# Kernel tuning notes

Measured on AMD Instinct MI355X. Metric: run time of the kernel, lower is better.

## Reference

```python
import jax, jax.numpy as jnp
import numpy as np

LORA_ALPHA = 2.0

def setup_inputs() -> dict:
    key = jax.random.key(0)
    k1, k2, k3, k4 = jax.random.split(key, 4)
    B, S, D_IN, D_OUT, R = 4, 2048, 4096, 4096, 16
    x = jax.random.normal(k1, (B, S, D_IN), dtype=jnp.float32)
    weight = jax.random.normal(k2, (D_OUT, D_IN), dtype=jnp.float32) * (1.0 / np.sqrt(D_IN))
    lora_A = jax.random.normal(k3, (R, D_IN), dtype=jnp.float32) * (1.0 / np.sqrt(D_IN))
    lora_B = jax.random.normal(k4, (D_OUT, R), dtype=jnp.float32) * 0.02
    return {"x": x, "weight": weight, "lora_A": lora_A, "lora_B": lora_B}

def reference(x, weight, lora_A, lora_B):
    # main_out = F.linear(x, weight) = x @ weight.T
    main_out = jnp.einsum('bsd,od->bso', x, weight)
    # Faithful to source: materialize lora_weight = B @ A (out x in), then full linear
    lora_weight = lora_B @ lora_A  # [out, in]
    lora_out = jnp.einsum('bsd,od->bso', x, lora_weight) * LORA_ALPHA
    return main_out + lora_out
```

## Files before the change

kernel.cpp:

```cpp
#include <hip/hip_runtime.h>
#include <stdint.h>

typedef __attribute__((ext_vector_type(8))) short bf16x8;
typedef __attribute__((ext_vector_type(4))) float f32x4;

#define GM 8192
#define GN 4096
#define GK 4096
#define KTILES (GK / 64)

__device__ __forceinline__ unsigned short f2bf(float f) {
  union { float f; unsigned int u; } c; c.f = f;
  unsigned int u = c.u;
  unsigned int r = u + 0x7FFFu + ((u >> 16) & 1u);
  return (unsigned short)(r >> 16);
}

__global__ __launch_bounds__(256) void cvt_x_kernel(const float* __restrict__ x,
                                                    unsigned short* __restrict__ xb) {
  int i = blockIdx.x * 256 + threadIdx.x;
  const float4* p = (const float4*)x + (size_t)i * 2;
  float4 a = p[0], b = p[1];
  unsigned short t[8] = { f2bf(a.x), f2bf(a.y), f2bf(a.z), f2bf(a.w),
                          f2bf(b.x), f2bf(b.y), f2bf(b.z), f2bf(b.w) };
  int4 pk; __builtin_memcpy(&pk, t, 16);
  ((int4*)xb)[i] = pk;
}

__global__ __launch_bounds__(256) void weff_kernel(const float* __restrict__ w,
                                                   const float* __restrict__ lA,
                                                   const float* __restrict__ lB,
                                                   unsigned short* __restrict__ wb) {
  const int K = GK;
  int idx = blockIdx.x * 256 + threadIdx.x;
  int cg = idx & 511;
  int rg = idx >> 9;
  int i0 = cg << 3;
  int o0 = rg << 3;

  float acc[8][8];
#pragma unroll
  for (int r = 0; r < 8; ++r)
#pragma unroll
    for (int c = 0; c < 8; ++c) acc[r][c] = 0.f;

#pragma unroll
  for (int r = 0; r < 16; ++r) {
    float4 a0 = *(const float4*)(lA + (size_t)r * K + i0);
    float4 a1 = *(const float4*)(lA + (size_t)r * K + i0 + 4);
    float av[8] = { a0.x, a0.y, a0.z, a0.w, a1.x, a1.y, a1.z, a1.w };
#pragma unroll
    for (int row = 0; row < 8; ++row) {
      float b = lB[(size_t)(o0 + row) * 16 + r];
#pragma unroll
      for (int c = 0; c < 8; ++c) acc[row][c] += b * av[c];
    }
  }

#pragma unroll
  for (int row = 0; row < 8; ++row) {
    float4 w0 = *(const float4*)(w + (size_t)(o0 + row) * K + i0);
    float4 w1 = *(const float4*)(w + (size_t)(o0 + row) * K + i0 + 4);
    unsigned short t[8] = {
      f2bf(w0.x + 2.0f * acc[row][0]), f2bf(w0.y + 2.0f * acc[row][1]),
      f2bf(w0.z + 2.0f * acc[row][2]), f2bf(w0.w + 2.0f * acc[row][3]),
      f2bf(w1.x + 2.0f * acc[row][4]), f2bf(w1.y + 2.0f * acc[row][5]),
      f2bf(w1.z + 2.0f * acc[row][6]), f2bf(w1.w + 2.0f * acc[row][7]) };
    int4 pk; __builtin_memcpy(&pk, t, 16);
    *(int4*)(wb + (size_t)(o0 + row) * K + i0) = pk;
  }
}


__device__ __forceinline__ void gload16(const unsigned short* g, char* l) {
  __builtin_amdgcn_global_load_lds((__attribute__((address_space(1))) void*)g,
                                   (__attribute__((address_space(3))) void*)l, 16, 0, 0);
}

__device__ __forceinline__ void bar() {
  asm volatile("" ::: "memory");
  __builtin_amdgcn_s_barrier();
  asm volatile("" ::: "memory");
}

template <int N>
__device__ __forceinline__ void vmwait() {
  if constexpr (N == 0)      asm volatile("s_waitcnt vmcnt(0)" ::: "memory");
  else if constexpr (N == 2) asm volatile("s_waitcnt vmcnt(2)" ::: "memory");
  else if constexpr (N == 4) asm volatile("s_waitcnt vmcnt(4)" ::: "memory");
  else if constexpr (N == 6) asm volatile("s_waitcnt vmcnt(6)" ::: "memory");
}

#define MFMA_BF16(a, b, c) __builtin_amdgcn_mfma_f32_16x16x32_bf16((a), (b), (c), 0, 0, 0)

template <int HALF>
__device__ __forceinline__ void stage_half(const unsigned short* A, const unsigned short* B,
                                           char* smem, int bm0, int bn0, int w, int lane,
                                           int kt, int buf) {
  int sr, isB;
  if constexpr (HALF == 0)      { sr = w + (w & 4);                   isB = 0; }
  else if constexpr (HALF == 1) { sr = ((w >> 1) << 2) + (w & 1);     isB = 1; }
  else if constexpr (HALF == 2) { sr = ((w >> 1) << 2) + (w & 1) + 2; isB = 1; }
  else                          { sr = w + (w & 4) + 4;               isB = 0; }
  const unsigned short* mat = isB ? B : A;
  const int grow = (isB ? bn0 : bm0) + sr * 16 + (lane >> 2);
  const int gcol = ((lane & 3) * 8) ^ ((lane & 32) ? 16 : 0);
#pragma unroll
  for (int sc = 0; sc < 2; ++sc) {
    const unsigned short* src = mat + (size_t)grow * GK + kt * 64 + sc * 32 + gcol;
    char* dst = smem + (buf << 16) + (isB ? 32768 : 0) + ((sr * 2 + sc) << 10);
    gload16(src, dst);
  }
}

__device__ __forceinline__ bf16x8 ldsA(const char* smem, int buf, int sr, int sc, int foff) {
  return *(const bf16x8*)(smem + (buf << 16) + ((sr * 2 + sc) << 10) + foff);
}
__device__ __forceinline__ bf16x8 ldsB(const char* smem, int buf, int sr, int sc, int foff) {
  return *(const bf16x8*)(smem + (buf << 16) + 32768 + ((sr * 2 + sc) << 10) + foff);
}

template <int CUR, int TAIL>
__device__ __forceinline__ void ktile_body(const unsigned short* __restrict__ A,
                                           const unsigned short* __restrict__ B,
                                           char* smem, int bm0, int bn0, int w, int lane,
                                           int wm, int wn, int foff, int kt,
                                           bf16x8 (&av)[4][2], bf16x8 (&bv0)[2][2],
                                           bf16x8 (&bv1)[2][2], f32x4 (&acc)[8][4]) {
  constexpr int NXT = CUR ^ 1;

#pragma unroll
  for (int mi = 0; mi < 4; ++mi) {
    av[mi][0] = ldsA(smem, CUR, wm * 8 + mi, 0, foff);
    av[mi][1] = ldsA(smem, CUR, wm * 8 + mi, 1, foff);
  }
#pragma unroll
  for (int ni = 0; ni < 2; ++ni) {
    bv0[ni][0] = ldsB(smem, CUR, wn * 4 + ni, 0, foff);
    bv0[ni][1] = ldsB(smem, CUR, wn * 4 + ni, 1, foff);
  }
  if constexpr (TAIL < 2) { stage_half<1>(A, B, smem, bm0, bn0, w, lane, kt + 1, NXT); vmwait<6>(); }
  else                    { vmwait<2>(); }
  bar();
  __builtin_amdgcn_s_setprio(1);
#pragma unroll
  for (int mi = 0; mi < 4; ++mi) {
    acc[mi][0] = MFMA_BF16(av[mi][0], bv0[0][0], acc[mi][0]);
    acc[mi][0] = MFMA_BF16(av[mi][1], bv0[0][1], acc[mi][0]);
    acc[mi][1] = MFMA_BF16(av[mi][0], bv0[1][0], acc[mi][1]);
    acc[mi][1] = MFMA_BF16(av[mi][1], bv0[1][1], acc[mi][1]);
  }
  __builtin_amdgcn_s_setprio(0);
  bar();

#pragma unroll
  for (int ni = 0; ni < 2; ++ni) {
    bv1[ni][0] = ldsB(smem, CUR, wn * 4 + 2 + ni, 0, foff);
    bv1[ni][1] = ldsB(smem, CUR, wn * 4 + 2 + ni, 1, foff);
  }
  if constexpr (TAIL < 2) { stage_half<2>(A, B, smem, bm0, bn0, w, lane, kt + 1, NXT); vmwait<6>(); }
  else                    { vmwait<0>(); }
  bar();
  __builtin_amdgcn_s_setprio(1);
#pragma unroll
  for (int mi = 0; mi < 4; ++mi) {
    acc[mi][2] = MFMA_BF16(av[mi][0], bv1[0][0], acc[mi][2]);
    acc[mi][2] = MFMA_BF16(av[mi][1], bv1[0][1], acc[mi][2]);
    acc[mi][3] = MFMA_BF16(av[mi][0], bv1[1][0], acc[mi][3]);
    acc[mi][3] = MFMA_BF16(av[mi][1], bv1[1][1], acc[mi][3]);
  }
  __builtin_amdgcn_s_setprio(0);
  bar();

#pragma unroll
  for (int mi = 0; mi < 4; ++mi) {
    av[mi][0] = ldsA(smem, CUR, wm * 8 + 4 + mi, 0, foff);
    av[mi][1] = ldsA(smem, CUR, wm * 8 + 4 + mi, 1, foff);
  }
  if constexpr (TAIL < 2) { stage_half<3>(A, B, smem, bm0, bn0, w, lane, kt + 1, NXT); vmwait<6>(); }
  bar();
  __builtin_amdgcn_s_setprio(1);
#pragma unroll
  for (int mi = 0; mi < 4; ++mi) {
    acc[4 + mi][2] = MFMA_BF16(av[mi][0], bv1[0][0], acc[4 + mi][2]);
    acc[4 + mi][2] = MFMA_BF16(av[mi][1], bv1[0][1], acc[4 + mi][2]);
    acc[4 + mi][3] = MFMA_BF16(av[mi][0], bv1[1][0], acc[4 + mi][3]);
    acc[4 + mi][3] = MFMA_BF16(av[mi][1], bv1[1][1], acc[4 + mi][3]);
  }
  __builtin_amdgcn_s_setprio(0);
  bar();

  if constexpr (TAIL == 0) {
    stage_half<0>(A, B, smem, bm0, bn0, w, lane, kt + 2, CUR);
    vmwait<6>();
  } else if constexpr (TAIL == 1) {
    vmwait<4>();
  }
  bar();
  __builtin_amdgcn_s_setprio(1);
#pragma unroll
  for (int mi = 0; mi < 4; ++mi) {
    acc[4 + mi][0] = MFMA_BF16(av[mi][0], bv0[0][0], acc[4 + mi][0]);
    acc[4 + mi][0] = MFMA_BF16(av[mi][1], bv0[0][1], acc[4 + mi][0]);
    acc[4 + mi][1] = MFMA_BF16(av[mi][0], bv0[1][0], acc[4 + mi][1]);
    acc[4 + mi][1] = MFMA_BF16(av[mi][1], bv0[1][1], acc[4 + mi][1]);
  }
  __builtin_amdgcn_s_setprio(0);
  bar();
}

__global__ __launch_bounds__(512, 2) void gemm_bt_kernel(const unsigned short* __restrict__ A,
                                                         const unsigned short* __restrict__ B,
                                                         float* __restrict__ C) {
  __shared__ alignas(16) char smem[131072];

  const int t = threadIdx.x, lane = t & 63, w = t >> 6;
  const int wm = w >> 2, wn = w & 3;

  const int bid = blockIdx.x;
  const int wg  = (bid & 7) * (512 / 8) + (bid >> 3);
  const int bx = wg & 15, by = wg >> 4;
  const int bm0 = by * 256, bn0 = bx * 256;

  int foff = (lane & 15) * 64 + ((lane >> 4) << 4);
  foff ^= ((foff >> 9) & 1) << 5;

  stage_half<0>(A, B, smem, bm0, bn0, w, lane, 0, 0);
  stage_half<1>(A, B, smem, bm0, bn0, w, lane, 0, 0);
  stage_half<2>(A, B, smem, bm0, bn0, w, lane, 0, 0);
  stage_half<3>(A, B, smem, bm0, bn0, w, lane, 0, 0);
  stage_half<0>(A, B, smem, bm0, bn0, w, lane, 1, 1);
  vmwait<6>();
  bar();

  f32x4 acc[8][4] = {};
  bf16x8 av[4][2], bv0[2][2], bv1[2][2];

  for (int kt = 0; kt < KTILES - 2; kt += 2) {
    ktile_body<0, 0>(A, B, smem, bm0, bn0, w, lane, wm, wn, foff, kt,     av, bv0, bv1, acc);
    ktile_body<1, 0>(A, B, smem, bm0, bn0, w, lane, wm, wn, foff, kt + 1, av, bv0, bv1, acc);
  }
  ktile_body<0, 1>(A, B, smem, bm0, bn0, w, lane, wm, wn, foff, KTILES - 2, av, bv0, bv1, acc);
  ktile_body<1, 2>(A, B, smem, bm0, bn0, w, lane, wm, wn, foff, KTILES - 1, av, bv0, bv1, acc);

  const int orow = (lane >> 4) << 2;
#pragma unroll
  for (int mi = 0; mi < 8; ++mi) {
#pragma unroll
    for (int ni = 0; ni < 4; ++ni) {
      float* cp = C + (size_t)(bm0 + wm * 128 + mi * 16 + orow) * GN
                    + (bn0 + wn * 64 + ni * 16 + (lane & 15));
#pragma unroll
      for (int r = 0; r < 4; ++r)
        cp[(size_t)r * GN] = acc[mi][ni][r];
    }
  }
}

extern "C" void kernel_launch(void* const* d_in, const int* in_sizes, int n_in,
                              void* d_out, int out_size, void* d_ws, size_t ws_size,
                              hipStream_t stream) {
  const float* x  = (const float*)d_in[0];
  const float* w  = (const float*)d_in[1];
  const float* lA = (const float*)d_in[2];
  const float* lB = (const float*)d_in[3];
  float* out = (float*)d_out;

  const int M = GM, N = GN, K = GK;

  unsigned short* xb = (unsigned short*)d_ws;
  unsigned short* wb = xb + (size_t)M * K;

  cvt_x_kernel<<<dim3((M * K / 8) / 256), dim3(256), 0, stream>>>(x, xb);
  weff_kernel<<<dim3((N / 8) * (K / 8) / 256), dim3(256), 0, stream>>>(w, lA, lB, wb);
  gemm_bt_kernel<<<dim3((M / 256) * (N / 256)), dim3(512), 0, stream>>>(xb, wb, out);
}
```

Baseline: 288.6 us.

## Restructure GEMM main loop into 4-buffer K=32 pipeline with one barrier per phase

Replaces the double-buffered K=64 tile schedule, which split each tile into four half-phases with two barriers each, with a four-slot ring of K=32 tiles. Each phase issues the global-to-LDS load for the tile two steps ahead, reads all A/B fragments for the current tile, waits on the older load, takes one barrier, then runs 32 MFMAs. The goal is fewer barriers per unit of work and a deeper prefetch, at the cost of smaller MFMA batches between syncs. LDS use falls from 128 KB to 128 KB split into four 32 KB slots.

```diff
diff --git a/kernel.cpp b/kernel.cpp
--- a/kernel.cpp
+++ b/kernel.cpp
@@ -7,7 +7,7 @@
 #define GM 8192
 #define GN 4096
 #define GK 4096
-#define KTILES (GK / 64)
+#define KT32 (GK / 32)
 
 __device__ __forceinline__ unsigned short f2bf(float f) {
   union { float f; unsigned int u; } c; c.f = f;
@@ -86,127 +86,60 @@
 template <int N>
 __device__ __forceinline__ void vmwait() {
   if constexpr (N == 0)      asm volatile("s_waitcnt vmcnt(0)" ::: "memory");
-  else if constexpr (N == 2) asm volatile("s_waitcnt vmcnt(2)" ::: "memory");
   else if constexpr (N == 4) asm volatile("s_waitcnt vmcnt(4)" ::: "memory");
-  else if constexpr (N == 6) asm volatile("s_waitcnt vmcnt(6)" ::: "memory");
 }
 
 #define MFMA_BF16(a, b, c) __builtin_amdgcn_mfma_f32_16x16x32_bf16((a), (b), (c), 0, 0, 0)
 
-template <int HALF>
-__device__ __forceinline__ void stage_half(const unsigned short* A, const unsigned short* B,
+template <int BUF>
+__device__ __forceinline__ void stage_tile(const unsigned short* A, const unsigned short* B,
                                            char* smem, int bm0, int bn0, int w, int lane,
-                                           int kt, int buf) {
-  int sr, isB;
-  if constexpr (HALF == 0)      { sr = w + (w & 4);                   isB = 0; }
-  else if constexpr (HALF == 1) { sr = ((w >> 1) << 2) + (w & 1);     isB = 1; }
-  else if constexpr (HALF == 2) { sr = ((w >> 1) << 2) + (w & 1) + 2; isB = 1; }
-  else                          { sr = w + (w & 4) + 4;               isB = 0; }
-  const unsigned short* mat = isB ? B : A;
-  const int grow = (isB ? bn0 : bm0) + sr * 16 + (lane >> 2);
+                                           int kt) {
   const int gcol = ((lane & 3) * 8) ^ ((lane & 32) ? 16 : 0);
-#pragma unroll
-  for (int sc = 0; sc < 2; ++sc) {
-    const unsigned short* src = mat + (size_t)grow * GK + kt * 64 + sc * 32 + gcol;
-    char* dst = smem + (buf << 16) + (isB ? 32768 : 0) + ((sr * 2 + sc) << 10);
-    gload16(src, dst);
-  }
-}
-
-__device__ __forceinline__ bf16x8 ldsA(const char* smem, int buf, int sr, int sc, int foff) {
-  return *(const bf16x8*)(smem + (buf << 16) + ((sr * 2 + sc) << 10) + foff);
-}
-__device__ __forceinline__ bf16x8 ldsB(const char* smem, int buf, int sr, int sc, int foff) {
-  return *(const bf16x8*)(smem + (buf << 16) + 32768 + ((sr * 2 + sc) << 10) + foff);
-}
-
-template <int CUR, int TAIL>
-__device__ __forceinline__ void ktile_body(const unsigned short* __restrict__ A,
-                                           const unsigned short* __restrict__ B,
-                                           char* smem, int bm0, int bn0, int w, int lane,
-                                           int wm, int wn, int foff, int kt,
-                                           bf16x8 (&av)[4][2], bf16x8 (&bv0)[2][2],
-                                           bf16x8 (&bv1)[2][2], f32x4 (&acc)[8][4]) {
-  constexpr int NXT = CUR ^ 1;
-
-#pragma unroll
-  for (int mi = 0; mi < 4; ++mi) {
-    av[mi][0] = ldsA(smem, CUR, wm * 8 + mi, 0, foff);
-    av[mi][1] = ldsA(smem, CUR, wm * 8 + mi, 1, foff);
-  }
-#pragma unroll
-  for (int ni = 0; ni < 2; ++ni) {
-    bv0[ni][0] = ldsB(smem, CUR, wn * 4 + ni, 0, foff);
-    bv0[ni][1] = ldsB(smem, CUR, wn * 4 + ni, 1, foff);
-  }
-  if constexpr (TAIL < 2) { stage_half<1>(A, B, smem, bm0, bn0, w, lane, kt + 1, NXT); vmwait<6>(); }
-  else                    { vmwait<2>(); }
+  const int r = lane >> 2;
+#pragma unroll
+  for (int i = 0; i < 2; ++i) {
+    const int sr = 2 * w + i;
+    gload16(A + (size_t)(bm0 + sr * 16 + r) * GK + kt * 32 + gcol,
+            smem + BUF * 32768 + (sr << 10));
+    gload16(B + (size_t)(bn0 + sr * 16 + r) * GK + kt * 32 + gcol,
+            smem + BUF * 32768 + 16384 + (sr << 10));
+  }
+}
+
+__device__ __forceinline__ bf16x8 ldsA(const char* smem, int buf, int sr, int foff) {
+  return *(const bf16x8*)(smem + buf * 32768 + (sr << 10) + foff);
+}
+__device__ __forceinline__ bf16x8 ldsB(const char* smem, int buf, int sr, int foff) {
+  return *(const bf16x8*)(smem + buf * 32768 + 16384 + (sr << 10) + foff);
+}
+
+template <int BUF, int TAIL>
+__device__ __forceinline__ void phase(const unsigned short* __restrict__ A,
+                                      const unsigned short* __restrict__ B,
+                                      char* smem, int bm0, int bn0, int w, int lane,
+                                      int wm, int wn, int foff, int kt,
+                                      f32x4 (&acc)[8][4]) {
+  if constexpr (TAIL == 0)
+    stage_tile<(BUF + 2) & 3>(A, B, smem, bm0, bn0, w, lane, kt + 2);
+
+  bf16x8 av[8], bv[4];
+#pragma unroll
+  for (int mi = 0; mi < 8; ++mi) av[mi] = ldsA(smem, BUF, wm * 8 + mi, foff);
+#pragma unroll
+  for (int ni = 0; ni < 4; ++ni) bv[ni] = ldsB(smem, BUF, wn * 4 + ni, foff);
+
+  if constexpr (TAIL == 0)      vmwait<4>();
+  else if constexpr (TAIL == 1) vmwait<0>();
   bar();
+
   __builtin_amdgcn_s_setprio(1);
 #pragma unroll
-  for (int mi = 0; mi < 4; ++mi) {
-    acc[mi][0] = MFMA_BF16(av[mi][0], bv0[0][0], acc[mi][0]);
-    acc[mi][0] = MFMA_BF16(av[mi][1], bv0[0][1], acc[mi][0]);
-    acc[mi][1] = MFMA_BF16(av[mi][0], bv0[1][0], acc[mi][1]);
-    acc[mi][1] = MFMA_BF16(av[mi][1], bv0[1][1], acc[mi][1]);
-  }
+  for (int mi = 0; mi < 8; ++mi)
+#pragma unroll
+    for (int ni = 0; ni < 4; ++ni)
+      acc[mi][ni] = MFMA_BF16(av[mi], bv[ni], acc[mi][ni]);
   __builtin_amdgcn_s_setprio(0);
-  bar();
-
-#pragma unroll
-  for (int ni = 0; ni < 2; ++ni) {
-    bv1[ni][0] = ldsB(smem, CUR, wn * 4 + 2 + ni, 0, foff);
-    bv1[ni][1] = ldsB(smem, CUR, wn * 4 + 2 + ni, 1, foff);
-  }
-  if constexpr (TAIL < 2) { stage_half<2>(A, B, smem, bm0, bn0, w, lane, kt + 1, NXT); vmwait<6>(); }
-  else                    { vmwait<0>(); }
-  bar();
-  __builtin_amdgcn_s_setprio(1);
-#pragma unroll
-  for (int mi = 0; mi < 4; ++mi) {
-    acc[mi][2] = MFMA_BF16(av[mi][0], bv1[0][0], acc[mi][2]);
-    acc[mi][2] = MFMA_BF16(av[mi][1], bv1[0][1], acc[mi][2]);
-    acc[mi][3] = MFMA_BF16(av[mi][0], bv1[1][0], acc[mi][3]);
-    acc[mi][3] = MFMA_BF16(av[mi][1], bv1[1][1], acc[mi][3]);
-  }
-  __builtin_amdgcn_s_setprio(0);
-  bar();
-
-#pragma unroll
-  for (int mi = 0; mi < 4; ++mi) {
-    av[mi][0] = ldsA(smem, CUR, wm * 8 + 4 + mi, 0, foff);
-    av[mi][1] = ldsA(smem, CUR, wm * 8 + 4 + mi, 1, foff);
-  }
-  if constexpr (TAIL < 2) { stage_half<3>(A, B, smem, bm0, bn0, w, lane, kt + 1, NXT); vmwait<6>(); }
-  bar();
-  __builtin_amdgcn_s_setprio(1);
-#pragma unroll
-  for (int mi = 0; mi < 4; ++mi) {
-    acc[4 + mi][2] = MFMA_BF16(av[mi][0], bv1[0][0], acc[4 + mi][2]);
-    acc[4 + mi][2] = MFMA_BF16(av[mi][1], bv1[0][1], acc[4 + mi][2]);
-    acc[4 + mi][3] = MFMA_BF16(av[mi][0], bv1[1][0], acc[4 + mi][3]);
-    acc[4 + mi][3] = MFMA_BF16(av[mi][1], bv1[1][1], acc[4 + mi][3]);
-  }
-  __builtin_amdgcn_s_setprio(0);
-  bar();
-
-  if constexpr (TAIL == 0) {
-    stage_half<0>(A, B, smem, bm0, bn0, w, lane, kt + 2, CUR);
-    vmwait<6>();
-  } else if constexpr (TAIL == 1) {
-    vmwait<4>();
-  }
-  bar();
-  __builtin_amdgcn_s_setprio(1);
-#pragma unroll
-  for (int mi = 0; mi < 4; ++mi) {
-    acc[4 + mi][0] = MFMA_BF16(av[mi][0], bv0[0][0], acc[4 + mi][0]);
-    acc[4 + mi][0] = MFMA_BF16(av[mi][1], bv0[0][1], acc[4 + mi][0]);
-    acc[4 + mi][1] = MFMA_BF16(av[mi][0], bv0[1][0], acc[4 + mi][1]);
-    acc[4 + mi][1] = MFMA_BF16(av[mi][1], bv0[1][1], acc[4 + mi][1]);
-  }
-  __builtin_amdgcn_s_setprio(0);
-  bar();
 }
 
 __global__ __launch_bounds__(512, 2) void gemm_bt_kernel(const unsigned short* __restrict__ A,
@@ -225,23 +158,23 @@
   int foff = (lane & 15) * 64 + ((lane >> 4) << 4);
   foff ^= ((foff >> 9) & 1) << 5;
 
-  stage_half<0>(A, B, smem, bm0, bn0, w, lane, 0, 0);
-  stage_half<1>(A, B, smem, bm0, bn0, w, lane, 0, 0);
-  stage_half<2>(A, B, smem, bm0, bn0, w, lane, 0, 0);
-  stage_half<3>(A, B, smem, bm0, bn0, w, lane, 0, 0);
-  stage_half<0>(A, B, smem, bm0, bn0, w, lane, 1, 1);
-  vmwait<6>();
+  stage_tile<0>(A, B, smem, bm0, bn0, w, lane, 0);
+  stage_tile<1>(A, B, smem, bm0, bn0, w, lane, 1);
+  vmwait<4>();
   bar();
 
   f32x4 acc[8][4] = {};
-  bf16x8 av[4][2], bv0[2][2], bv1[2][2];
-
-  for (int kt = 0; kt < KTILES - 2; kt += 2) {
-    ktile_body<0, 0>(A, B, smem, bm0, bn0, w, lane, wm, wn, foff, kt,     av, bv0, bv1, acc);
-    ktile_body<1, 0>(A, B, smem, bm0, bn0, w, lane, wm, wn, foff, kt + 1, av, bv0, bv1, acc);
-  }
-  ktile_body<0, 1>(A, B, smem, bm0, bn0, w, lane, wm, wn, foff, KTILES - 2, av, bv0, bv1, acc);
-  ktile_body<1, 2>(A, B, smem, bm0, bn0, w, lane, wm, wn, foff, KTILES - 1, av, bv0, bv1, acc);
+
+  for (int kt = 0; kt < KT32 - 4; kt += 4) {
+    phase<0, 0>(A, B, smem, bm0, bn0, w, lane, wm, wn, foff, kt,     acc);
+    phase<1, 0>(A, B, smem, bm0, bn0, w, lane, wm, wn, foff, kt + 1, acc);
+    phase<2, 0>(A, B, smem, bm0, bn0, w, lane, wm, wn, foff, kt + 2, acc);
+    phase<3, 0>(A, B, smem, bm0, bn0, w, lane, wm, wn, foff, kt + 3, acc);
+  }
+  phase<0, 0>(A, B, smem, bm0, bn0, w, lane, wm, wn, foff, KT32 - 4, acc);
+  phase<1, 0>(A, B, smem, bm0, bn0, w, lane, wm, wn, foff, KT32 - 3, acc);
+  phase<2, 1>(A, B, smem, bm0, bn0, w, lane, wm, wn, foff, KT32 - 2, acc);
+  phase<3, 2>(A, B, smem, bm0, bn0, w, lane, wm, wn, foff, KT32 - 1, acc);
 
   const int orow = (lane >> 4) << 2;
 #pragma unroll
```

After: 293.6 us. No clear change (+1.7%).

## Restructure GEMM prefetch schedule with deeper global-to-LDS lookahead and explicit lgkm waits

Applied to the files above, without the earlier changes.

Reorders the global_load_lds staging so three quarter-tiles of the next k-tile are issued in the prologue. Each phase now issues its prefetch before its LDS reads, and only one vmcnt wait remains per k-tile instead of one per phase. Explicit lgkmcnt waits are added around barriers so LDS reads can overlap the barrier. This aims to cut per-phase global-load stalls and barrier latency, but it depends on subtle buffer-reuse ordering that could introduce races.

```diff
diff --git a/kernel.cpp b/kernel.cpp
--- a/kernel.cpp
+++ b/kernel.cpp
@@ -86,17 +86,22 @@
 template <int N>
 __device__ __forceinline__ void vmwait() {
   if constexpr (N == 0)      asm volatile("s_waitcnt vmcnt(0)" ::: "memory");
-  else if constexpr (N == 2) asm volatile("s_waitcnt vmcnt(2)" ::: "memory");
-  else if constexpr (N == 4) asm volatile("s_waitcnt vmcnt(4)" ::: "memory");
   else if constexpr (N == 6) asm volatile("s_waitcnt vmcnt(6)" ::: "memory");
 }
 
+__device__ __forceinline__ void lgkm0() {
+  asm volatile("s_waitcnt lgkmcnt(0)" ::: "memory");
+}
+__device__ __forceinline__ void lgkm8() {
+  asm volatile("s_waitcnt lgkmcnt(8)" ::: "memory");
+}
+
 #define MFMA_BF16(a, b, c) __builtin_amdgcn_mfma_f32_16x16x32_bf16((a), (b), (c), 0, 0, 0)
 
-template <int HALF>
+template <int HALF, int BUF>
 __device__ __forceinline__ void stage_half(const unsigned short* A, const unsigned short* B,
                                            char* smem, int bm0, int bn0, int w, int lane,
-                                           int kt, int buf) {
+                                           int kt) {
   int sr, isB;
   if constexpr (HALF == 0)      { sr = w + (w & 4);                   isB = 0; }
   else if constexpr (HALF == 1) { sr = ((w >> 1) << 2) + (w & 1);     isB = 1; }
@@ -108,27 +113,28 @@
 #pragma unroll
   for (int sc = 0; sc < 2; ++sc) {
     const unsigned short* src = mat + (size_t)grow * GK + kt * 64 + sc * 32 + gcol;
-    char* dst = smem + (buf << 16) + (isB ? 32768 : 0) + ((sr * 2 + sc) << 10);
+    char* dst = smem + BUF * 65536 + (isB ? 32768 : 0) + ((sr * 2 + sc) << 10);
     gload16(src, dst);
   }
 }
 
 __device__ __forceinline__ bf16x8 ldsA(const char* smem, int buf, int sr, int sc, int foff) {
-  return *(const bf16x8*)(smem + (buf << 16) + ((sr * 2 + sc) << 10) + foff);
+  return *(const bf16x8*)(smem + buf * 65536 + ((sr * 2 + sc) << 10) + foff);
 }
 __device__ __forceinline__ bf16x8 ldsB(const char* smem, int buf, int sr, int sc, int foff) {
-  return *(const bf16x8*)(smem + (buf << 16) + 32768 + ((sr * 2 + sc) << 10) + foff);
+  return *(const bf16x8*)(smem + buf * 65536 + 32768 + ((sr * 2 + sc) << 10) + foff);
 }
 
 template <int CUR, int TAIL>
-__device__ __forceinline__ void ktile_body(const unsigned short* __restrict__ A,
-                                           const unsigned short* __restrict__ B,
-                                           char* smem, int bm0, int bn0, int w, int lane,
-                                           int wm, int wn, int foff, int kt,
-                                           bf16x8 (&av)[4][2], bf16x8 (&bv0)[2][2],
-                                           bf16x8 (&bv1)[2][2], f32x4 (&acc)[8][4]) {
+__device__ __forceinline__ void ktile(const unsigned short* __restrict__ A,
+                                      const unsigned short* __restrict__ B,
+                                      char* smem, int bm0, int bn0, int w, int lane,
+                                      int wm, int wn, int foff, int kt,
+                                      bf16x8 (&av)[4][2], bf16x8 (&bv0)[2][2],
+                                      bf16x8 (&bv1)[2][2], f32x4 (&acc)[8][4]) {
   constexpr int NXT = CUR ^ 1;
 
+  if constexpr (TAIL < 2) stage_half<3, NXT>(A, B, smem, bm0, bn0, w, lane, kt + 1);
 #pragma unroll
   for (int mi = 0; mi < 4; ++mi) {
     av[mi][0] = ldsA(smem, CUR, wm * 8 + mi, 0, foff);
@@ -139,9 +145,9 @@
     bv0[ni][0] = ldsB(smem, CUR, wn * 4 + ni, 0, foff);
     bv0[ni][1] = ldsB(smem, CUR, wn * 4 + ni, 1, foff);
   }
-  if constexpr (TAIL < 2) { stage_half<1>(A, B, smem, bm0, bn0, w, lane, kt + 1, NXT); vmwait<6>(); }
-  else                    { vmwait<2>(); }
-  bar();
+  lgkm8();
+  bar();
+  lgkm0();
   __builtin_amdgcn_s_setprio(1);
 #pragma unroll
   for (int mi = 0; mi < 4; ++mi) {
@@ -153,14 +159,14 @@
   __builtin_amdgcn_s_setprio(0);
   bar();
 
+  if constexpr (TAIL == 0) stage_half<0, CUR>(A, B, smem, bm0, bn0, w, lane, kt + 2);
 #pragma unroll
   for (int ni = 0; ni < 2; ++ni) {
     bv1[ni][0] = ldsB(smem, CUR, wn * 4 + 2 + ni, 0, foff);
     bv1[ni][1] = ldsB(smem, CUR, wn * 4 + 2 + ni, 1, foff);
   }
-  if constexpr (TAIL < 2) { stage_half<2>(A, B, smem, bm0, bn0, w, lane, kt + 1, NXT); vmwait<6>(); }
-  else                    { vmwait<0>(); }
-  bar();
+  bar();
+  lgkm0();
   __builtin_amdgcn_s_setprio(1);
 #pragma unroll
   for (int mi = 0; mi < 4; ++mi) {
@@ -172,13 +178,14 @@
   __builtin_amdgcn_s_setprio(0);
   bar();
 
+  if constexpr (TAIL == 0) stage_half<1, CUR>(A, B, smem, bm0, bn0, w, lane, kt + 2);
 #pragma unroll
   for (int mi = 0; mi < 4; ++mi) {
     av[mi][0] = ldsA(smem, CUR, wm * 8 + 4 + mi, 0, foff);
     av[mi][1] = ldsA(smem, CUR, wm * 8 + 4 + mi, 1, foff);
   }
-  if constexpr (TAIL < 2) { stage_half<3>(A, B, smem, bm0, bn0, w, lane, kt + 1, NXT); vmwait<6>(); }
-  bar();
+  bar();
+  lgkm0();
   __builtin_amdgcn_s_setprio(1);
 #pragma unroll
   for (int mi = 0; mi < 4; ++mi) {
@@ -191,10 +198,10 @@
   bar();
 
   if constexpr (TAIL == 0) {
-    stage_half<0>(A, B, smem, bm0, bn0, w, lane, kt + 2, CUR);
+    stage_half<2, CUR>(A, B, smem, bm0, bn0, w, lane, kt + 2);
     vmwait<6>();
   } else if constexpr (TAIL == 1) {
-    vmwait<4>();
+    vmwait<0>();
   }
   bar();
   __builtin_amdgcn_s_setprio(1);
@@ -225,23 +232,25 @@
   int foff = (lane & 15) * 64 + ((lane >> 4) << 4);
   foff ^= ((foff >> 9) & 1) << 5;
 
-  stage_half<0>(A, B, smem, bm0, bn0, w, lane, 0, 0);
-  stage_half<1>(A, B, smem, bm0, bn0, w, lane, 0, 0);
-  stage_half<2>(A, B, smem, bm0, bn0, w, lane, 0, 0);
-  stage_half<3>(A, B, smem, bm0, bn0, w, lane, 0, 0);
-  stage_half<0>(A, B, smem, bm0, bn0, w, lane, 1, 1);
+  stage_half<0, 0>(A, B, smem, bm0, bn0, w, lane, 0);
+  stage_half<1, 0>(A, B, smem, bm0, bn0, w, lane, 0);
+  stage_half<2, 0>(A, B, smem, bm0, bn0, w, lane, 0);
+  stage_half<3, 0>(A, B, smem, bm0, bn0, w, lane, 0);
+  stage_half<0, 1>(A, B, smem, bm0, bn0, w, lane, 1);
+  stage_half<1, 1>(A, B, smem, bm0, bn0, w, lane, 1);
+  stage_half<2, 1>(A, B, smem, bm0, bn0, w, lane, 1);
   vmwait<6>();
   bar();
 
   f32x4 acc[8][4] = {};
   bf16x8 av[4][2], bv0[2][2], bv1[2][2];
 
-  for (int kt = 0; kt < KTILES - 2; kt += 2) {
-    ktile_body<0, 0>(A, B, smem, bm0, bn0, w, lane, wm, wn, foff, kt,     av, bv0, bv1, acc);
-    ktile_body<1, 0>(A, B, smem, bm0, bn0, w, lane, wm, wn, foff, kt + 1, av, bv0, bv1, acc);
-  }
-  ktile_body<0, 1>(A, B, smem, bm0, bn0, w, lane, wm, wn, foff, KTILES - 2, av, bv0, bv1, acc);
-  ktile_body<1, 2>(A, B, smem, bm0, bn0, w, lane, wm, wn, foff, KTILES - 1, av, bv0, bv1, acc);
+  for (int kt = 0; kt + 2 <= KTILES - 2; kt += 2) {
+    ktile<0, 0>(A, B, smem, bm0, bn0, w, lane, wm, wn, foff, kt,     av, bv0, bv1, acc);
+    ktile<1, 0>(A, B, smem, bm0, bn0, w, lane, wm, wn, foff, kt + 1, av, bv0, bv1, acc);
+  }
+  ktile<0, 1>(A, B, smem, bm0, bn0, w, lane, wm, wn, foff, KTILES - 2, av, bv0, bv1, acc);
+  ktile<1, 2>(A, B, smem, bm0, bn0, w, lane, wm, wn, foff, KTILES - 1, av, bv0, bv1, acc);
 
   const int orow = (lane >> 4) << 2;
 #pragma unroll
```

New measurement: 288.5 us. About the same (-0.0%).
